# Performance work log

Hardware: AMD Instinct MI355X
Metric: run time of the kernel (lower is better)

The kernel has to match this reference:

```python
import jax, jax.numpy as jnp
import numpy as np

# SOM hyperparameters (from init_kwargs)
M_ROWS = 64
N_COLS = 64
DIM = 256
MAX_EPOCHS = 100
INITIAL_RADIUS = 32.0  # max(m, n) / 2
INITIAL_LR = 0.1
STD_COEFF = 0.5
BATCH = 8192

# [m*n, 2] integer grid locations (constant, non-differentiable)
_LOC_VECTS = jnp.asarray(
    np.stack(np.meshgrid(np.arange(M_ROWS), np.arange(N_COLS), indexing='ij'), axis=-1).reshape(-1, 2),
    dtype=jnp.int32,
)


def setup_inputs() -> dict:
    key = jax.random.key(0)
    k1, k2 = jax.random.split(key)
    return {
        'input_vect': jax.random.normal(k1, (BATCH, DIM), dtype=jnp.float32),
        'weights': jax.random.normal(k2, (M_ROWS * N_COLS, DIM), dtype=jnp.float32),
        'epoch': 10,
    }


def reference(input_vect, weights, epoch):
    # squared_distance[b, m] = sum_d (weights[m, d] - x[b, d])^2  -> [B, M]
    sq_dist = (
        jnp.sum(input_vect * input_vect, axis=1, keepdims=True)
        - 2.0 * (input_vect @ weights.T)
        + jnp.sum(weights * weights, axis=1)[None, :]
    )
    bmu_indices = jnp.argmin(sq_dist, axis=1)             # [B]
    bmu_locs = _LOC_VECTS[bmu_indices]                    # [B, 2]

    ep = jnp.float32(epoch)
    radius = INITIAL_RADIUS - ep * ((INITIAL_RADIUS - 1.0) / (MAX_EPOCHS - 1.0))
    alpha = INITIAL_LR * (1.0 - ep / MAX_EPOCHS)

    # bmu_distance_squares[b, m] = ||locs[m] - bmu_locs[b]||^2  -> [B, M]
    diff = _LOC_VECTS[None, :, :] - bmu_locs[:, None, :]  # int [B, M, 2]
    bmu_dist_sq = jnp.sum(diff * diff, axis=2).astype(jnp.float32)

    denom_nf = 2.0 * jnp.square(radius * STD_COEFF)
    learning_rate_op = jnp.exp(-bmu_dist_sq / denom_nf) * alpha  # [B, M]

    # numerator[m, d] = sum_b lr[b, m] * x[b, d]
    numerator = jnp.einsum('bm,bd->md', learning_rate_op, input_vect)
    denominator = jnp.sum(learning_rate_op, axis=0)[:, None] + 1e-12  # [M, 1]
    new_weights = numerator / denominator
    return bmu_locs, new_weights
```

## Files before the change

kernel.cpp:

```cpp
#include <hip/hip_runtime.h>
#include <stdint.h>

#define DIM   256
#define BATCH 8192
#define MCELL 4096

typedef unsigned long long u64;
typedef unsigned short u16;
typedef __attribute__((ext_vector_type(8))) short bf16x8;
typedef __attribute__((ext_vector_type(4))) float f32x4;

__device__ __forceinline__ u64 packMin(float v, unsigned idx) {
    unsigned u = __float_as_uint(v);
    u = (u & 0x80000000u) ? ~u : (u | 0x80000000u);
    return ((u64)u << 32) | (u64)idx;
}
__device__ __forceinline__ u16 f2bf(float f) {
    unsigned u = __float_as_uint(f);
    u += 0x7fffu + ((u >> 16) & 1u);
    return (u16)(u >> 16);
}
__device__ __forceinline__ void gll16(const void* g, const char* l) {
    __builtin_amdgcn_global_load_lds(
        (const __attribute__((address_space(1))) unsigned int*)g,
        (__attribute__((address_space(3))) unsigned int*)l, 16, 0, 0);
}
__device__ __forceinline__ u64 umin64(u64 a, u64 b) { return a < b ? a : b; }
__device__ __forceinline__ u64 umax64(u64 a, u64 b) { return a < b ? b : a; }
__device__ __forceinline__ void ins2(u64& t1, u64& t2, u64 p) {
    u64 hi = umax64(p, t1);
    t1 = umin64(p, t1);
    t2 = umin64(t2, hi);
}
__device__ __forceinline__ void merge2(u64& a1, u64& a2, u64 o1, u64 o2) {
    u64 H1 = umax64(a1, o1);
    a1 = umin64(a1, o1);
    a2 = umin64(H1, umin64(a2, o2));
}
__device__ __forceinline__ void merge3(u64& a1, u64& a2, u64& a3,
                                       u64 o1, u64 o2, u64 o3) {
    u64 L1 = umin64(a1, o1), H1 = umax64(a1, o1);
    u64 L2 = umin64(a2, o2);
    u64 L3 = umin64(a3, o3);
    a1 = L1;
    a2 = umin64(H1, L2);
    a3 = umin64(umax64(H1, L2), L3);
}

__global__ void k_prep(const float* __restrict__ X, const float* __restrict__ W,
                       u16* __restrict__ Xh, u16* __restrict__ Wh,
                       float* __restrict__ w2, const int* __restrict__ epoch_p,
                       float* __restrict__ scal) {
    const int blk = blockIdx.x;
    const int t = threadIdx.x;
    if (blk == 3072) {
        int raw = epoch_p[0];
        float ep = (raw >= 0 && raw < 100000) ? (float)raw : __int_as_float(raw);
        float radius = 32.0f - ep * (31.0f / 99.0f);
        float alpha  = 0.1f * (1.0f - ep / 100.0f);
        float rs = radius * 0.5f;
        float denom = 2.0f * rs * rs;
        if (t < 64)       scal[t]  = expf(-((float)(t * t)) / denom);
        else if (t == 64) scal[64] = alpha;
        return;
    }
    if (blk < 2048) {
        const int fi = blk * 256 + t;
        float4 v = ((const float4*)X)[fi];
        ushort4 h = {f2bf(v.x), f2bf(v.y), f2bf(v.z), f2bf(v.w)};
        ((ushort4*)Xh)[fi] = h;
    } else {
        const int fi = (blk - 2048) * 256 + t;
        float4 v = ((const float4*)W)[fi];
        ushort4 h = {f2bf(v.x), f2bf(v.y), f2bf(v.z), f2bf(v.w)};
        ((ushort4*)Wh)[fi] = h;
        float s = v.x * v.x + v.y * v.y + v.z * v.z + v.w * v.w;
        #pragma unroll
        for (int off = 32; off; off >>= 1) s += __shfl_down(s, off);
        if ((t & 63) == 0) w2[fi >> 6] = s;
    }
}

__global__ __launch_bounds__(256, 3)
void k_gemm_argmin(const u16* __restrict__ Xh, const u16* __restrict__ Wh,
                   const float* __restrict__ w2, u64* __restrict__ slots) {
    __shared__ char smem[49152];
    const int wg = blockIdx.x;
    const int swz = (wg & 7) * 256 + (wg >> 3);
    const int bt = swz >> 5;
    const int mt = swz & 31;
    const int tid = threadIdx.x;
    const int wid = tid >> 6;
    const int lane = tid & 63;
    const int wr = wid >> 1, wc = wid & 1;
    const int b0 = bt * 128, m0 = mt * 128;

    const int sr0 = wid * 32 + (lane >> 2);
    const int sr1 = sr0 + 16;
    const int ss  = lane & 3;
    const int sg0 = ss ^ ((sr0 >> 1) & 3);
    const int sg1 = ss ^ ((sr1 >> 1) & 3);
    const size_t gA0 = (size_t)(b0 + sr0) * DIM + sg0 * 8;
    const size_t gA1 = (size_t)(b0 + sr1) * DIM + sg1 * 8;
    const size_t gB0 = (size_t)(m0 + sr0) * DIM + sg0 * 8;
    const size_t gB1 = (size_t)(m0 + sr1) * DIM + sg1 * 8;
    const int ldsA = wid * 2048;

    const int rl = lane & 15, g = lane >> 4;
    const int slot = g ^ ((rl >> 1) & 3);
    const int xoff = (wc * 64 + rl) * 64 + slot * 16;
    const int woff = (wr * 64 + rl) * 64 + slot * 16;

    f32x4 acc[4][4];
    #pragma unroll
    for (int i = 0; i < 4; ++i)
        #pragma unroll
        for (int j = 0; j < 4; ++j) acc[i][j] = (f32x4){0.f, 0.f, 0.f, 0.f};

    #define STAGE(buf, c) do {                                                \
        char* base_ = smem + (buf) * 16384;                                   \
        const int co_ = (c) * 32;                                             \
        gll16(Xh + gA0 + co_, base_ + ldsA);                                  \
        gll16(Xh + gA1 + co_, base_ + ldsA + 1024);                           \
        gll16(Wh + gB0 + co_, base_ + 8192 + ldsA);                           \
        gll16(Wh + gB1 + co_, base_ + 8192 + ldsA + 1024);                    \
    } while (0)

    STAGE(0, 0);
    STAGE(1, 1);
    #pragma unroll
    for (int c = 0; c < 8; ++c) {
        if (c < 6) {
            STAGE((c + 2) % 3, c + 2);
            asm volatile("s_waitcnt vmcnt(8)" ::: "memory");
        } else if (c == 6) {
            asm volatile("s_waitcnt vmcnt(4)" ::: "memory");
        } else {
            asm volatile("s_waitcnt vmcnt(0)" ::: "memory");
        }
        __builtin_amdgcn_sched_barrier(0);
        __builtin_amdgcn_s_barrier();

        const char* bufc = smem + (c % 3) * 16384;
        bf16x8 wf[4];
        #pragma unroll
        for (int i = 0; i < 4; ++i)
            wf[i] = *(const bf16x8*)(bufc + 8192 + woff + i * 1024);
        __builtin_amdgcn_s_setprio(1);
        #pragma unroll
        for (int j = 0; j < 4; ++j) {
            const bf16x8 xf = *(const bf16x8*)(bufc + xoff + j * 1024);
            #pragma unroll
            for (int i = 0; i < 4; ++i)
                acc[i][j] = __builtin_amdgcn_mfma_f32_16x16x32_bf16(wf[i], xf, acc[i][j], 0, 0, 0);
        }
        __builtin_amdgcn_s_setprio(0);
        __builtin_amdgcn_s_barrier();
    }
    #undef STAGE

    float w2v[16];
    #pragma unroll
    for (int ii = 0; ii < 16; ++ii)
        w2v[ii] = w2[m0 + wr * 64 + (ii >> 2) * 16 + g * 4 + (ii & 3)];

    __syncthreads();
    u64* ex = (u64*)smem;

    #pragma unroll
    for (int j = 0; j < 4; ++j) {
        u64 t1 = ~0ull, t2 = ~0ull;
        #pragma unroll
        for (int i = 0; i < 4; ++i)
            #pragma unroll
            for (int q = 0; q < 4; ++q) {
                const float d = fmaf(-2.0f, acc[i][j][q], w2v[i * 4 + q]);
                ins2(t1, t2, packMin(d, (unsigned)(m0 + wr * 64 + i * 16 + g * 4 + q)));
            }
        #pragma unroll
        for (int off = 16; off <= 32; off <<= 1) {
            const u64 o1 = __shfl_xor(t1, off);
            const u64 o2 = __shfl_xor(t2, off);
            merge2(t1, t2, o1, o2);
        }
        if (lane < 16) {
            u64* e = ex + ((size_t)(wc * 64 + j * 16 + rl) * 2 + wr) * 2;
            e[0] = t1; e[1] = t2;
        }
    }
    __syncthreads();
    if (tid < 128) {
        const u64* e = ex + (size_t)tid * 4;
        u64 a1 = e[0], a2 = e[1];
        merge2(a1, a2, e[2], e[3]);
        slots[(size_t)(b0 + tid) * 64 + mt]      = a1;
        slots[(size_t)(b0 + tid) * 64 + 32 + mt] = a2;
    }
}

__global__ void k_merge(const u64* __restrict__ slots, const float* __restrict__ X,
                        const float* __restrict__ W, const float* __restrict__ w2,
                        float* __restrict__ out_locs, float* __restrict__ A,
                        float* __restrict__ cnt) {
    const int wid = threadIdx.x >> 6, l = threadIdx.x & 63;
    const int row = blockIdx.x * 4 + wid;
    u64 t1 = slots[(size_t)row * 64 + l], t2 = ~0ull, t3 = ~0ull;
    #pragma unroll
    for (int off = 1; off <= 32; off <<= 1) {
        const u64 o1 = __shfl_xor(t1, off);
        const u64 o2 = __shfl_xor(t2, off);
        const u64 o3 = __shfl_xor(t3, off);
        merge3(t1, t2, t3, o1, o2, o3);
    }
    const int cand[3] = {(int)(t1 & 0xFFFFFFFFull), (int)(t2 & 0xFFFFFFFFull),
                         (int)(t3 & 0xFFFFFFFFull)};
    const float4 xv = *(const float4*)(X + (size_t)row * DIM + l * 4);
    float bd = 0.0f; int bm = -1;
    #pragma unroll
    for (int tix = 0; tix < 3; ++tix) {
        const int mc = cand[tix];
        const float4 wv = *(const float4*)(W + (size_t)mc * DIM + l * 4);
        float s = xv.x * wv.x + xv.y * wv.y + xv.z * wv.z + xv.w * wv.w;
        #pragma unroll
        for (int off = 1; off <= 32; off <<= 1) s += __shfl_xor(s, off);
        const float d = w2[mc] - 2.0f * s;
        if (bm < 0 || d < bd || (d == bd && mc < bm)) { bd = d; bm = mc; }
    }
    if (l == 0) {
        out_locs[row * 2 + 0] = (float)(bm >> 6);
        out_locs[row * 2 + 1] = (float)(bm & 63);
        atomicAdd(&cnt[bm], 1.0f);
    }
    float* ap = A + (size_t)bm * DIM + l * 4;
    atomicAdd(ap + 0, xv.x);
    atomicAdd(ap + 1, xv.y);
    atomicAdd(ap + 2, xv.z);
    atomicAdd(ap + 3, xv.w);
}

__global__ void k_conv1(const float* __restrict__ A, const float* __restrict__ E,
                        float* __restrict__ T1, const float* __restrict__ cnt,
                        float* __restrict__ c1) {
    if (blockIdx.x >= 4096) {
        int t = (blockIdx.x - 4096) * 256 + threadIdx.x;
        int gi = t >> 6, mj = t & 63;
        float acc = 0.0f;
        #pragma unroll
        for (int gj = 0; gj < 64; ++gj) {
            int dd = mj - gj; dd = dd < 0 ? -dd : dd;
            acc += E[dd] * cnt[gi * 64 + gj];
        }
        c1[gi * 64 + mj] = acc;
        return;
    }
    __shared__ float Es[64];
    const int d = threadIdx.x;
    if (d < 64) Es[d] = E[d];
    __syncthreads();
    const int gi = blockIdx.x >> 6, mj = blockIdx.x & 63;
    const float* base = A + (size_t)gi * 64 * DIM + d;
    float acc = 0.0f;
    #pragma unroll
    for (int gj = 0; gj < 64; ++gj) {
        int dd = mj - gj; dd = dd < 0 ? -dd : dd;
        acc += Es[dd] * base[(size_t)gj * DIM];
    }
    T1[(size_t)blockIdx.x * DIM + d] = acc;
}

__global__ void k_conv2(const float* __restrict__ T1, const float* __restrict__ scal,
                        const float* __restrict__ c1, float* __restrict__ outw) {
    __shared__ float Es[64];
    __shared__ float salpha;
    const int d = threadIdx.x;
    if (d < 64) Es[d] = scal[d];
    if (d == 64) salpha = scal[64];
    __syncthreads();
    const int mi = blockIdx.x >> 6, mj = blockIdx.x & 63;
    float acc = 0.0f, den = 0.0f;
    #pragma unroll
    for (int gi = 0; gi < 64; ++gi) {
        int dd = mi - gi; dd = dd < 0 ? -dd : dd;
        acc += Es[dd] * T1[((size_t)gi * 64 + mj) * DIM + d];
        den += Es[dd] * c1[gi * 64 + mj];
    }
    const float a = salpha;
    const float v = (a * acc) / (a * den + 1e-12f);
    outw[((size_t)mi * 64 + mj) * DIM + d] = v;
}

extern "C" void kernel_launch(void* const* d_in, const int* in_sizes, int n_in,
                              void* d_out, int out_size, void* d_ws, size_t ws_size,
                              hipStream_t stream) {
    const float* X = (const float*)d_in[0];
    const float* W = (const float*)d_in[1];
    const int*   ep = (const int*)d_in[2];
    float* out = (float*)d_out;

    char* ws = (char*)d_ws;
    u64*   slots = (u64*)(ws + 0);
    float* T1    = (float*)(ws + 0);
    u16*   Xh    = (u16*)(ws + (4u << 20));
    float* A     = (float*)(ws + (4u << 20));
    float* cnt   = (float*)(ws + (8u << 20));
    u16*   Wh    = (u16*)(ws + (8u << 20) + 16384);
    float* w2    = (float*)(ws + (10u << 20) + 16384);
    float* scal  = (float*)(ws + (10u << 20) + 32768);
    float* c1    = (float*)(ws + (10u << 20) + 36864);

    k_prep<<<3073, 256, 0, stream>>>(X, W, Xh, Wh, w2, ep, scal);
    k_gemm_argmin<<<2048, 256, 0, stream>>>(Xh, Wh, w2, slots);
    hipMemsetAsync(ws + (4u << 20), 0, (4u << 20) + 16384, stream);
    k_merge<<<2048, 256, 0, stream>>>(slots, X, W, w2, out, A, cnt);
    k_conv1<<<4112, 256, 0, stream>>>(A, scal, T1, cnt, c1);
    k_conv2<<<4096, 256, 0, stream>>>(T1, scal, c1, out + 16384);
}
```

Baseline: 172.8 us.

## Replace atomic scatter-accumulate with per-cell gather over BMU assignments

k_merge now writes only the BMU index per row instead of doing float atomics into the per-cell accumulator and count. A new k_gather kernel has each block scan all BMU indices, build a shared list of matching rows, and sum their input vectors. This removes the memset and the global atomic traffic. In exchange, every block reads the whole BMU array, and the large shared list limits occupancy.

```diff
diff --git a/kernel.cpp b/kernel.cpp
--- a/kernel.cpp
+++ b/kernel.cpp
@@ -200,8 +200,7 @@
 
 __global__ void k_merge(const u64* __restrict__ slots, const float* __restrict__ X,
                         const float* __restrict__ W, const float* __restrict__ w2,
-                        float* __restrict__ out_locs, float* __restrict__ A,
-                        float* __restrict__ cnt) {
+                        float* __restrict__ out_locs, int* __restrict__ bmu) {
     const int wid = threadIdx.x >> 6, l = threadIdx.x & 63;
     const int row = blockIdx.x * 4 + wid;
     u64 t1 = slots[(size_t)row * 64 + l], t2 = ~0ull, t3 = ~0ull;
@@ -229,13 +228,30 @@
     if (l == 0) {
         out_locs[row * 2 + 0] = (float)(bm >> 6);
         out_locs[row * 2 + 1] = (float)(bm & 63);
-        atomicAdd(&cnt[bm], 1.0f);
-    }
-    float* ap = A + (size_t)bm * DIM + l * 4;
-    atomicAdd(ap + 0, xv.x);
-    atomicAdd(ap + 1, xv.y);
-    atomicAdd(ap + 2, xv.z);
-    atomicAdd(ap + 3, xv.w);
+        bmu[row] = bm;
+    }
+}
+
+__global__ void k_gather(const int* __restrict__ bmu, const float* __restrict__ X,
+                         float* __restrict__ A, float* __restrict__ cnt) {
+    __shared__ int n;
+    __shared__ int lst[BATCH];
+    const int m = blockIdx.x;
+    const int t = threadIdx.x;
+    if (t == 0) n = 0;
+    __syncthreads();
+    #pragma unroll
+    for (int i = 0; i < BATCH / 256; ++i) {
+        const int r = i * 256 + t;
+        if (bmu[r] == m) lst[atomicAdd(&n, 1)] = r;
+    }
+    __syncthreads();
+    const int nn = n;
+    float acc = 0.0f;
+    for (int k = 0; k < nn; ++k)
+        acc += X[(size_t)lst[k] * DIM + t];
+    A[(size_t)m * DIM + t] = acc;
+    if (t == 0) cnt[m] = (float)nn;
 }
 
 __global__ void k_conv1(const float* __restrict__ A, const float* __restrict__ E,
@@ -307,11 +323,12 @@
     float* w2    = (float*)(ws + (10u << 20) + 16384);
     float* scal  = (float*)(ws + (10u << 20) + 32768);
     float* c1    = (float*)(ws + (10u << 20) + 36864);
+    int*   bmu   = (int*)(ws + (10u << 20) + 53248);
 
     k_prep<<<3073, 256, 0, stream>>>(X, W, Xh, Wh, w2, ep, scal);
     k_gemm_argmin<<<2048, 256, 0, stream>>>(Xh, Wh, w2, slots);
-    hipMemsetAsync(ws + (4u << 20), 0, (4u << 20) + 16384, stream);
-    k_merge<<<2048, 256, 0, stream>>>(slots, X, W, w2, out, A, cnt);
+    k_merge<<<2048, 256, 0, stream>>>(slots, X, W, w2, out, bmu);
+    k_gather<<<MCELL, 256, 0, stream>>>(bmu, X, A, cnt);
     k_conv1<<<4112, 256, 0, stream>>>(A, scal, T1, cnt, c1);
     k_conv2<<<4096, 256, 0, stream>>>(T1, scal, c1, out + 16384);
 }
```

Measured after the change: 163.1 us. -5.6%, faster.
